# Kernel tuning notes

Hardware: AMD Instinct MI355X
Metric: run time of the kernel (lower is better)

## Reference

```python
import jax, jax.numpy as jnp
import numpy as np

UNITS = 1024
OUT_STEPS = 200
SEQ_LEN = 5
NUM_FEATURES = 1
BATCH = 4096


def _lstm_cell(x, h, c, kernel, recurrent_kernel, bias):
    # Keras LSTMCell: z = x@K + h@R + b, gates in order i, f, g(candidate), o
    z = x @ kernel + h @ recurrent_kernel + bias  # [B, 4U]
    i, f, g, o = jnp.split(z, 4, axis=-1)
    i = jax.nn.sigmoid(i)
    f = jax.nn.sigmoid(f)
    g = jnp.tanh(g)
    o = jax.nn.sigmoid(o)
    c_new = f * c + i * g
    h_new = o * jnp.tanh(c_new)
    return h_new, c_new


def setup_inputs() -> dict:
    key = jax.random.key(0)
    ks = jax.random.split(key, 8)
    s = 0.05  # modest init scale to keep gates unsaturated
    return {
        "inputs": jax.random.normal(ks[0], (BATCH, SEQ_LEN, NUM_FEATURES), jnp.float32),
        "kernel": jax.random.normal(ks[1], (NUM_FEATURES, 4 * UNITS), jnp.float32) * s,
        "recurrent_kernel": jax.random.normal(ks[2], (UNITS, 4 * UNITS), jnp.float32) * s,
        "bias": jax.random.normal(ks[3], (4 * UNITS,), jnp.float32) * s,
        "w1": jax.random.normal(ks[4], (UNITS, NUM_FEATURES), jnp.float32) * s,
        "b1": jax.random.normal(ks[5], (NUM_FEATURES,), jnp.float32) * s,
        "w2": jax.random.normal(ks[6], (NUM_FEATURES, NUM_FEATURES), jnp.float32) * s,
        "b2": jax.random.normal(ks[7], (NUM_FEATURES,), jnp.float32) * s,
    }


def reference(inputs, kernel, recurrent_kernel, bias, w1, b1, w2, b2):
    B = inputs.shape[0]
    h0 = jnp.zeros((B, UNITS), inputs.dtype)
    c0 = jnp.zeros((B, UNITS), inputs.dtype)

    # warmup: run LSTM over the input sequence (lax.scan over time)
    def warm_step(carry, x_t):
        h, c = carry
        h, c = _lstm_cell(x_t, h, c, kernel, recurrent_kernel, bias)
        return (h, c), None

    (h, c), _ = jax.lax.scan(warm_step, (h0, c0), jnp.swapaxes(inputs, 0, 1))
    pred0 = jax.nn.relu(h @ w1 + b1)  # first prediction: dense1 only (per warmup())

    def dec_step(carry, _):
        pred, h, c = carry
        h, c = _lstm_cell(pred, h, c, kernel, recurrent_kernel, bias)
        x = jax.nn.relu(h @ w1 + b1)
        pred = x @ w2 + b2
        return (pred, h, c), pred

    _, preds = jax.lax.scan(dec_step, (pred0, h, c), None, length=OUT_STEPS - 1)
    # preds: [T-1, B, F] -> stack with pred0 and transpose to [B, T, F]
    all_preds = jnp.concatenate([pred0[None], preds], axis=0)
    return jnp.transpose(all_preds, (1, 0, 2))
```

## Files before the change

kernel.cpp:

```cpp
#include <hip/hip_runtime.h>
#include <hip/hip_bf16.h>
#include <stdint.h>
#include <stddef.h>

#define B_SZ   4096
#define U_SZ   1024
#define SEQ    5
#define TSTEPS 200
#define STEPS  204

typedef __bf16 bf16_t;
typedef __bf16 bf16x8 __attribute__((ext_vector_type(8)));
typedef float  f32x4  __attribute__((ext_vector_type(4)));

#define AS1 __attribute__((address_space(1)))
#define AS3 __attribute__((address_space(3)))

#define LOAD_LDS16(gp, lp) \
    __builtin_amdgcn_global_load_lds((const AS1 unsigned int*)(gp), \
                                     (AS3 unsigned int*)(lp), 16, 0, 0)

__device__ __forceinline__ float fsig(float x) {
    return 1.0f / (1.0f + __expf(-x));
}
__device__ __forceinline__ float ftanh(float x) {
    x = fminf(fmaxf(x, -15.0f), 15.0f);
    float e = __expf(2.0f * x);
    return (e - 1.0f) / (e + 1.0f);
}

__global__ void pack_R(const float* __restrict__ R, bf16_t* __restrict__ Rp) {
    int idx = blockIdx.x * 256 + threadIdx.x;
    int e    = idx & 7;
    int slot = (idx >> 3) & 3;
    int c    = (idx >> 5) & 127;
    int kb   = (idx >> 12) & 31;
    int ub   = idx >> 17;
    int g  = (c >> 4) & 3;
    int wc = c >> 6;
    int cl = c & 15;
    int n  = g * 1024 + ub * 32 + wc * 16 + cl;
    int k  = kb * 32 + ((slot ^ ((c >> 1) & 3)) << 3) + e;
    Rp[idx] = (bf16_t)R[(size_t)k * 4096 + n];
}

__global__ __launch_bounds__(256, 2)
void lstm_step(const bf16_t* __restrict__ hin,
               bf16_t* __restrict__ hout,
               float* __restrict__ cst,
               const bf16_t* __restrict__ Rp,
               const float* __restrict__ Wx,
               const float* __restrict__ bias,
               const float* __restrict__ w1,
               const float* __restrict__ b1,
               const float* __restrict__ w2,
               const float* __restrict__ b2,
               const float* __restrict__ inputs,
               float* __restrict__ praw,
               float* __restrict__ out,
               int t)
{
    __shared__ __align__(16) bf16_t lsA[3][4096];
    __shared__ __align__(16) bf16_t lsB[3][2][4096];
    __shared__ float lsX[128];

    const int tid  = threadIdx.x;
    const int wave = tid >> 6;
    const int lane = tid & 63;
    const int p    = blockIdx.x;
    const int G    = blockIdx.y;
    const int l15  = lane & 15;
    const int quad = lane >> 4;
    const int rbase = (wave >> 1) * 64;
    const int wc    = wave & 1;
    const int a_kk32 = (((lane & 3) ^ ((lane >> 3) & 3)) << 3);
    const int sw32   = ((quad ^ ((l15 >> 1) & 3)) << 3);

    float*       pr_acc  = praw + (size_t)(t % 3) * B_SZ;
    const float* pr_read = praw + (size_t)((t + 2) % 3) * B_SZ;
    float*       pr_zero = praw + (size_t)((t + 1) % 3) * B_SZ;

    const bf16_t* Ap  = hin + (size_t)G * 128 * U_SZ;
    const bf16_t* Bp0 = Rp + (size_t)(2 * p) * 131072;
    const bf16_t* Bp1 = Bp0 + 131072;

    if (tid < 128) {
        int row = G * 128 + tid;
        float x;
        if (t < SEQ) {
            x = inputs[row * SEQ + t];
        } else {
            float x1 = fmaxf(pr_read[row] + b1[0], 0.f);
            x = (t == SEQ) ? x1 : x1 * w2[0] + b2[0];
            if (p == 0) out[(size_t)row * TSTEPS + (t - SEQ)] = x;
        }
        lsX[tid] = x;
        if (p == 0) pr_zero[row] = 0.f;
    }

    auto STAGE = [&](int ksrc, int buf) {
        #pragma unroll
        for (int i = 0; i < 2; ++i) {
            int brow = i * 64 + wave * 16;
            LOAD_LDS16(Ap + (size_t)(brow + (lane >> 2)) * U_SZ
                          + ksrc * 32 + a_kk32,
                       &lsA[buf][brow * 32]);
        }
        #pragma unroll
        for (int i = 0; i < 2; ++i) {
            int chunk = wave * 2 + i;
            LOAD_LDS16(Bp0 + (size_t)ksrc * 4096 + chunk * 512 + lane * 8,
                       &lsB[buf][0][chunk * 512]);
            LOAD_LDS16(Bp1 + (size_t)ksrc * 4096 + chunk * 512 + lane * 8,
                       &lsB[buf][1][chunk * 512]);
        }
    };

    STAGE(0, 0);
    STAGE(1, 1);

    f32x4 acc[2][4][4] = {};
    int bi = 0;

    for (int kb = 0; kb < 32; ++kb) {
        asm volatile("s_waitcnt vmcnt(6)" ::: "memory");
        __builtin_amdgcn_sched_barrier(0);
        __builtin_amdgcn_s_barrier();
        __builtin_amdgcn_sched_barrier(0);

        int bs = bi + 2; if (bs >= 3) bs -= 3;
        STAGE((kb + 2) & 31, bs);

        bf16x8 af[4], bfr[2][4];
        #pragma unroll
        for (int mi = 0; mi < 4; ++mi)
            af[mi] = *(const bf16x8*)
                &lsA[bi][(rbase + mi * 16 + l15) * 32 + sw32];
        #pragma unroll
        for (int T = 0; T < 2; ++T)
            #pragma unroll
            for (int ni = 0; ni < 4; ++ni)
                bfr[T][ni] = *(const bf16x8*)
                    &lsB[bi][T][(wc * 64 + ni * 16 + l15) * 32 + sw32];

        __builtin_amdgcn_s_setprio(1);
        #pragma unroll
        for (int T = 0; T < 2; ++T)
            #pragma unroll
            for (int mi = 0; mi < 4; ++mi)
                #pragma unroll
                for (int ni = 0; ni < 4; ++ni)
                    acc[T][mi][ni] = __builtin_amdgcn_mfma_f32_16x16x32_bf16(
                        af[mi], bfr[T][ni], acc[T][mi][ni], 0, 0, 0);
        __builtin_amdgcn_s_setprio(0);

        bi = bi + 1; if (bi >= 3) bi = 0;
    }

    int uu[2];
    uu[0] = (2 * p) * 32 + wc * 16 + l15;
    uu[1] = uu[0] + 32;
    float g_b[2][4], g_w[2][4], w1u[2];
    #pragma unroll
    for (int T = 0; T < 2; ++T) {
        #pragma unroll
        for (int g = 0; g < 4; ++g) {
            g_b[T][g] = bias[g * 1024 + uu[T]];
            g_w[T][g] = Wx[g * 1024 + uu[T]];
        }
        w1u[T] = w1[uu[T]];
    }
    const bool do_pred = (t >= SEQ - 1);

    #pragma unroll
    for (int mi = 0; mi < 4; ++mi) {
        #pragma unroll
        for (int r = 0; r < 4; ++r) {
            int rl   = rbase + mi * 16 + quad * 4 + r;
            int brow = G * 128 + rl;
            float xv = lsX[rl];
            float ps = 0.f;
            #pragma unroll
            for (int T = 0; T < 2; ++T) {
                float zi = acc[T][mi][0][r] + g_b[T][0] + xv * g_w[T][0];
                float zf = acc[T][mi][1][r] + g_b[T][1] + xv * g_w[T][1];
                float zg = acc[T][mi][2][r] + g_b[T][2] + xv * g_w[T][2];
                float zo = acc[T][mi][3][r] + g_b[T][3] + xv * g_w[T][3];
                float ig = fsig(zi), fg = fsig(zf);
                float gg = ftanh(zg), og = fsig(zo);
                size_t off = (size_t)brow * U_SZ + uu[T];
                float cn = fg * cst[off] + ig * gg;
                cst[off] = cn;
                float hv = og * ftanh(cn);
                hout[off] = (bf16_t)hv;
                ps += hv * w1u[T];
            }
            if (do_pred) {
                ps += __shfl_xor(ps, 1);
                ps += __shfl_xor(ps, 2);
                ps += __shfl_xor(ps, 4);
                ps += __shfl_xor(ps, 8);
                if (l15 == 0) atomicAdd(&pr_acc[brow], ps);
            }
        }
    }
}

__global__ void pred_final(const float* __restrict__ praw,
                           const float* __restrict__ b1,
                           const float* __restrict__ w2,
                           const float* __restrict__ b2,
                           float* __restrict__ out)
{
    int row = blockIdx.x * 256 + threadIdx.x;
    float x1 = fmaxf(praw[2 * B_SZ + row] + b1[0], 0.f);
    out[(size_t)row * TSTEPS + 199] = x1 * w2[0] + b2[0];
}

extern "C" void kernel_launch(void* const* d_in, const int* in_sizes, int n_in,
                              void* d_out, int out_size, void* d_ws, size_t ws_size,
                              hipStream_t stream) {
    const float* inputs = (const float*)d_in[0];
    const float* Wx     = (const float*)d_in[1];
    const float* R      = (const float*)d_in[2];
    const float* bias   = (const float*)d_in[3];
    const float* w1     = (const float*)d_in[4];
    const float* b1     = (const float*)d_in[5];
    const float* w2     = (const float*)d_in[6];
    const float* b2     = (const float*)d_in[7];
    float* out = (float*)d_out;

    char* ws = (char*)d_ws;
    const size_t RP_BYTES = (size_t)32 * 131072 * 2;
    const size_t H_BYTES  = (size_t)B_SZ * U_SZ * 2;
    const size_t C_BYTES  = (size_t)B_SZ * U_SZ * 4;
    bf16_t* Rp   = (bf16_t*)ws;                ws += RP_BYTES;
    bf16_t* h0   = (bf16_t*)ws;                ws += H_BYTES;
    bf16_t* h1   = (bf16_t*)ws;                ws += H_BYTES;
    float*  cbuf = (float*)ws;                 ws += C_BYTES;
    float*  praw = (float*)ws;                 ws += 3 * B_SZ * 4;
    bf16_t* hb[2] = {h0, h1};

    hipMemsetAsync(h0, 0, H_BYTES, stream);
    hipMemsetAsync(cbuf, 0, C_BYTES, stream);
    hipMemsetAsync(praw, 0, 3 * B_SZ * 4, stream);

    pack_R<<<16384, 256, 0, stream>>>(R, Rp);

    dim3 grid(16, 32);
    int cur = 0;
    for (int t = 0; t < STEPS; ++t) {
        lstm_step<<<grid, 256, 0, stream>>>(hb[cur], hb[1 - cur], cbuf, Rp,
                                            Wx, bias, w1, b1, w2, b2,
                                            inputs, praw, out, t);
        cur ^= 1;
    }
    pred_final<<<16, 256, 0, stream>>>(praw, b1, w2, b2, out);
}
```

Before: 9.719 ms.

## Register double-buffer LDS fragments and decouple A/B staging depths in GEMM loop

The K-loop now handles two k-blocks per iteration and keeps two register sets of A/B fragments. The next block's LDS reads are issued before the current block's MFMAs, so LDS latency overlaps matrix math. The B tiles drop from triple to double buffering in LDS, while A keeps three buffers and is prefetched one block further ahead. The vmcnt/lgkmcnt waits are reworked to match. This cuts LDS use and stalls between barrier and MFMA, at the cost of more vector registers and a more fragile wait-count schedule.

```diff
diff --git a/kernel.cpp b/kernel.cpp
--- a/kernel.cpp
+++ b/kernel.cpp
@@ -61,7 +61,7 @@
                int t)
 {
     __shared__ __align__(16) bf16_t lsA[3][4096];
-    __shared__ __align__(16) bf16_t lsB[3][2][4096];
+    __shared__ __align__(16) bf16_t lsB[2][2][4096];
     __shared__ float lsX[128];
 
     const int tid  = threadIdx.x;
@@ -98,63 +98,91 @@
         if (p == 0) pr_zero[row] = 0.f;
     }
 
-    auto STAGE = [&](int ksrc, int buf) {
+    auto STAGE_A = [&](int ksrc, int abuf) {
         #pragma unroll
         for (int i = 0; i < 2; ++i) {
             int brow = i * 64 + wave * 16;
             LOAD_LDS16(Ap + (size_t)(brow + (lane >> 2)) * U_SZ
                           + ksrc * 32 + a_kk32,
-                       &lsA[buf][brow * 32]);
-        }
+                       &lsA[abuf][brow * 32]);
+        }
+    };
+    auto STAGE_B = [&](int ksrc, int bbuf) {
         #pragma unroll
         for (int i = 0; i < 2; ++i) {
             int chunk = wave * 2 + i;
             LOAD_LDS16(Bp0 + (size_t)ksrc * 4096 + chunk * 512 + lane * 8,
-                       &lsB[buf][0][chunk * 512]);
+                       &lsB[bbuf][0][chunk * 512]);
             LOAD_LDS16(Bp1 + (size_t)ksrc * 4096 + chunk * 512 + lane * 8,
-                       &lsB[buf][1][chunk * 512]);
+                       &lsB[bbuf][1][chunk * 512]);
         }
     };
 
-    STAGE(0, 0);
-    STAGE(1, 1);
+#define DSREAD(abuf, bbuf, af, b0, b1)                                        \
+    {   _Pragma("unroll")                                                     \
+        for (int mi = 0; mi < 4; ++mi)                                        \
+            af[mi] = *(const bf16x8*)                                         \
+                &lsA[abuf][(rbase + mi * 16 + l15) * 32 + sw32];              \
+        _Pragma("unroll")                                                     \
+        for (int ni = 0; ni < 4; ++ni) {                                      \
+            b0[ni] = *(const bf16x8*)                                         \
+                &lsB[bbuf][0][(wc * 64 + ni * 16 + l15) * 32 + sw32];         \
+            b1[ni] = *(const bf16x8*)                                         \
+                &lsB[bbuf][1][(wc * 64 + ni * 16 + l15) * 32 + sw32];         \
+        } }
+
+#define MFMA32(af, b0, b1)                                                    \
+    {   __builtin_amdgcn_s_setprio(1);                                        \
+        _Pragma("unroll")                                                     \
+        for (int mi = 0; mi < 4; ++mi)                                        \
+            _Pragma("unroll")                                                 \
+            for (int ni = 0; ni < 4; ++ni)                                    \
+                acc[0][mi][ni] = __builtin_amdgcn_mfma_f32_16x16x32_bf16(     \
+                    af[mi], b0[ni], acc[0][mi][ni], 0, 0, 0);                 \
+        _Pragma("unroll")                                                     \
+        for (int mi = 0; mi < 4; ++mi)                                        \
+            _Pragma("unroll")                                                 \
+            for (int ni = 0; ni < 4; ++ni)                                    \
+                acc[1][mi][ni] = __builtin_amdgcn_mfma_f32_16x16x32_bf16(     \
+                    af[mi], b1[ni], acc[1][mi][ni], 0, 0, 0);                 \
+        __builtin_amdgcn_s_setprio(0); }
+
+#define SYNC_HALF                                                             \
+    asm volatile("s_waitcnt vmcnt(2) lgkmcnt(0)" ::: "memory");               \
+    __builtin_amdgcn_sched_barrier(0);                                        \
+    __builtin_amdgcn_s_barrier();                                             \
+    __builtin_amdgcn_sched_barrier(0);
+
+    STAGE_B(0, 0); STAGE_B(1, 1);
+    STAGE_A(0, 0); STAGE_A(1, 1); STAGE_A(2, 2);
 
     f32x4 acc[2][4][4] = {};
-    int bi = 0;
-
-    for (int kb = 0; kb < 32; ++kb) {
-        asm volatile("s_waitcnt vmcnt(6)" ::: "memory");
-        __builtin_amdgcn_sched_barrier(0);
-        __builtin_amdgcn_s_barrier();
-        __builtin_amdgcn_sched_barrier(0);
-
-        int bs = bi + 2; if (bs >= 3) bs -= 3;
-        STAGE((kb + 2) & 31, bs);
-
-        bf16x8 af[4], bfr[2][4];
-        #pragma unroll
-        for (int mi = 0; mi < 4; ++mi)
-            af[mi] = *(const bf16x8*)
-                &lsA[bi][(rbase + mi * 16 + l15) * 32 + sw32];
-        #pragma unroll
-        for (int T = 0; T < 2; ++T)
-            #pragma unroll
-            for (int ni = 0; ni < 4; ++ni)
-                bfr[T][ni] = *(const bf16x8*)
-                    &lsB[bi][T][(wc * 64 + ni * 16 + l15) * 32 + sw32];
-
-        __builtin_amdgcn_s_setprio(1);
-        #pragma unroll
-        for (int T = 0; T < 2; ++T)
-            #pragma unroll
-            for (int mi = 0; mi < 4; ++mi)
-                #pragma unroll
-                for (int ni = 0; ni < 4; ++ni)
-                    acc[T][mi][ni] = __builtin_amdgcn_mfma_f32_16x16x32_bf16(
-                        af[mi], bfr[T][ni], acc[T][mi][ni], 0, 0, 0);
-        __builtin_amdgcn_s_setprio(0);
-
-        bi = bi + 1; if (bi >= 3) bi = 0;
+    bf16x8 afE[4], bE0[4], bE1[4];
+    bf16x8 afO[4], bO0[4], bO1[4];
+
+    asm volatile("s_waitcnt vmcnt(2)" ::: "memory");
+    __builtin_amdgcn_s_barrier();
+    DSREAD(0, 0, afE, bE0, bE1);
+
+    int a = 0;
+    #pragma clang loop unroll(disable)
+    for (int kb = 0; kb < 32; kb += 2) {
+        const int a1 = (a + 1 == 3) ? 0 : a + 1;
+        const int a2 = (a1 + 1 == 3) ? 0 : a1 + 1;
+
+        SYNC_HALF;
+        STAGE_B((kb + 2) & 31, 0);
+        STAGE_A((kb + 3) & 31, a);
+        DSREAD(a1, 1, afO, bO0, bO1);
+        MFMA32(afE, bE0, bE1);
+
+        SYNC_HALF;
+        STAGE_B((kb + 3) & 31, 1);
+        STAGE_A((kb + 4) & 31, a1);
+        if (kb < 30) DSREAD(a2, 0, afE, bE0, bE1);
+        MFMA32(afO, bO0, bO1);
+
+        a = a2;
     }
 
     int uu[2];
```

Result: no change. 9.904 ms (+1.9%).

## Halve per-block N tile, double grid, and remap blocks for XCD-local L2 reuse

Applied to the files above, without the earlier changes.

Each block now computes one 32-unit slice of R instead of two, so the grid doubles to 1024 blocks and launch bounds rise to 4 blocks per CU. The B buffer drops to double buffering with staggered A/B staging, and lsX is replaced by a per-wave register read through shuffles. Block IDs are swizzled so that blocks on the same XCD share h rows and R columns, which should improve L2 hit rates. Smaller tiles lower arithmetic intensity per A load and add extra A traffic in exchange for more occupancy and parallelism.

```diff
diff --git a/kernel.cpp b/kernel.cpp
--- a/kernel.cpp
+++ b/kernel.cpp
@@ -44,7 +44,7 @@
     Rp[idx] = (bf16_t)R[(size_t)k * 4096 + n];
 }
 
-__global__ __launch_bounds__(256, 2)
+__global__ __launch_bounds__(256, 4)
 void lstm_step(const bf16_t* __restrict__ hin,
                bf16_t* __restrict__ hout,
                float* __restrict__ cst,
@@ -61,14 +61,16 @@
                int t)
 {
     __shared__ __align__(16) bf16_t lsA[3][4096];
-    __shared__ __align__(16) bf16_t lsB[3][2][4096];
-    __shared__ float lsX[128];
+    __shared__ __align__(16) bf16_t lsB[2][4096];
 
     const int tid  = threadIdx.x;
     const int wave = tid >> 6;
     const int lane = tid & 63;
-    const int p    = blockIdx.x;
-    const int G    = blockIdx.y;
+    const int bid  = blockIdx.x + 32 * blockIdx.y;
+    const int xcd  = bid & 7;
+    const int j    = bid >> 3;
+    const int p    = (xcd & 3) * 8 + (j & 7);
+    const int G    = (xcd >> 2) * 16 + (j >> 3);
     const int l15  = lane & 15;
     const int quad = lane >> 4;
     const int rbase = (wave >> 1) * 64;
@@ -80,96 +82,89 @@
     const float* pr_read = praw + (size_t)((t + 2) % 3) * B_SZ;
     float*       pr_zero = praw + (size_t)((t + 1) % 3) * B_SZ;
 
-    const bf16_t* Ap  = hin + (size_t)G * 128 * U_SZ;
-    const bf16_t* Bp0 = Rp + (size_t)(2 * p) * 131072;
-    const bf16_t* Bp1 = Bp0 + 131072;
-
-    if (tid < 128) {
-        int row = G * 128 + tid;
+    const bf16_t* Ap = hin + (size_t)G * 128 * U_SZ;
+    const bf16_t* Bp = Rp + (size_t)p * 131072;
+
+    auto STAGE_A = [&](int ksrc, int abuf) {
+        #pragma unroll
+        for (int i = 0; i < 2; ++i) {
+            int brow = i * 64 + wave * 16;
+            LOAD_LDS16(Ap + (size_t)(brow + (lane >> 2)) * U_SZ
+                          + ksrc * 32 + a_kk32,
+                       &lsA[abuf][brow * 32]);
+        }
+    };
+    auto STAGE_B = [&](int ksrc, int bbuf) {
+        #pragma unroll
+        for (int i = 0; i < 2; ++i) {
+            int chunk = wave * 2 + i;
+            LOAD_LDS16(Bp + (size_t)ksrc * 4096 + chunk * 512 + lane * 8,
+                       &lsB[bbuf][chunk * 512]);
+        }
+    };
+
+    STAGE_A(0, 0); STAGE_B(0, 0); STAGE_A(1, 1);
+
+    float xw;
+    {
+        int row = G * 128 + rbase + lane;
         float x;
         if (t < SEQ) {
             x = inputs[row * SEQ + t];
         } else {
             float x1 = fmaxf(pr_read[row] + b1[0], 0.f);
             x = (t == SEQ) ? x1 : x1 * w2[0] + b2[0];
-            if (p == 0) out[(size_t)row * TSTEPS + (t - SEQ)] = x;
-        }
-        lsX[tid] = x;
-        if (p == 0) pr_zero[row] = 0.f;
-    }
-
-    auto STAGE = [&](int ksrc, int buf) {
-        #pragma unroll
-        for (int i = 0; i < 2; ++i) {
-            int brow = i * 64 + wave * 16;
-            LOAD_LDS16(Ap + (size_t)(brow + (lane >> 2)) * U_SZ
-                          + ksrc * 32 + a_kk32,
-                       &lsA[buf][brow * 32]);
-        }
-        #pragma unroll
-        for (int i = 0; i < 2; ++i) {
-            int chunk = wave * 2 + i;
-            LOAD_LDS16(Bp0 + (size_t)ksrc * 4096 + chunk * 512 + lane * 8,
-                       &lsB[buf][0][chunk * 512]);
-            LOAD_LDS16(Bp1 + (size_t)ksrc * 4096 + chunk * 512 + lane * 8,
-                       &lsB[buf][1][chunk * 512]);
-        }
-    };
-
-    STAGE(0, 0);
-    STAGE(1, 1);
-
-    f32x4 acc[2][4][4] = {};
-    int bi = 0;
-
+            if (p == 0 && (wave & 1) == 0)
+                out[(size_t)row * TSTEPS + (t - SEQ)] = x;
+        }
+        xw = x;
+        if (p == 0 && (wave & 1) == 0) pr_zero[row] = 0.f;
+    }
+
+    f32x4 acc[4][4] = {};
+    int ap = 0;
+
+    #pragma clang loop unroll(disable)
     for (int kb = 0; kb < 32; ++kb) {
-        asm volatile("s_waitcnt vmcnt(6)" ::: "memory");
+        asm volatile("s_waitcnt vmcnt(2)" ::: "memory");
         __builtin_amdgcn_sched_barrier(0);
         __builtin_amdgcn_s_barrier();
         __builtin_amdgcn_sched_barrier(0);
 
-        int bs = bi + 2; if (bs >= 3) bs -= 3;
-        STAGE((kb + 2) & 31, bs);
-
-        bf16x8 af[4], bfr[2][4];
+        if (kb < 31) STAGE_B(kb + 1, (kb + 1) & 1);
+        int ap2 = ap + 2; if (ap2 >= 3) ap2 -= 3;
+        if (kb < 30) STAGE_A(kb + 2, ap2);
+
+        bf16x8 af[4], bfr[4];
         #pragma unroll
         for (int mi = 0; mi < 4; ++mi)
             af[mi] = *(const bf16x8*)
-                &lsA[bi][(rbase + mi * 16 + l15) * 32 + sw32];
-        #pragma unroll
-        for (int T = 0; T < 2; ++T)
+                &lsA[ap][(rbase + mi * 16 + l15) * 32 + sw32];
+        #pragma unroll
+        for (int ni = 0; ni < 4; ++ni)
+            bfr[ni] = *(const bf16x8*)
+                &lsB[kb & 1][(wc * 64 + ni * 16 + l15) * 32 + sw32];
+
+        __builtin_amdgcn_s_setprio(1);
+        #pragma unroll
+        for (int mi = 0; mi < 4; ++mi)
             #pragma unroll
             for (int ni = 0; ni < 4; ++ni)
-                bfr[T][ni] = *(const bf16x8*)
-                    &lsB[bi][T][(wc * 64 + ni * 16 + l15) * 32 + sw32];
-
-        __builtin_amdgcn_s_setprio(1);
-        #pragma unroll
-        for (int T = 0; T < 2; ++T)
-            #pragma unroll
-            for (int mi = 0; mi < 4; ++mi)
-                #pragma unroll
-                for (int ni = 0; ni < 4; ++ni)
-                    acc[T][mi][ni] = __builtin_amdgcn_mfma_f32_16x16x32_bf16(
-                        af[mi], bfr[T][ni], acc[T][mi][ni], 0, 0, 0);
+                acc[mi][ni] = __builtin_amdgcn_mfma_f32_16x16x32_bf16(
+                    af[mi], bfr[ni], acc[mi][ni], 0, 0, 0);
         __builtin_amdgcn_s_setprio(0);
 
-        bi = bi + 1; if (bi >= 3) bi = 0;
-    }
-
-    int uu[2];
-    uu[0] = (2 * p) * 32 + wc * 16 + l15;
-    uu[1] = uu[0] + 32;
-    float g_b[2][4], g_w[2][4], w1u[2];
+        ap = ap + 1; if (ap >= 3) ap = 0;
+    }
+
+    const int uu = p * 32 + wc * 16 + l15;
+    float g_b[4], g_w[4];
     #pragma unroll
-    for (int T = 0; T < 2; ++T) {
-        #pragma unroll
-        for (int g = 0; g < 4; ++g) {
-            g_b[T][g] = bias[g * 1024 + uu[T]];
-            g_w[T][g] = Wx[g * 1024 + uu[T]];
-        }
-        w1u[T] = w1[uu[T]];
-    }
+    for (int g = 0; g < 4; ++g) {
+        g_b[g] = bias[g * 1024 + uu];
+        g_w[g] = Wx[g * 1024 + uu];
+    }
+    const float w1u = w1[uu];
     const bool do_pred = (t >= SEQ - 1);
 
     #pragma unroll
@@ -178,23 +173,19 @@
         for (int r = 0; r < 4; ++r) {
             int rl   = rbase + mi * 16 + quad * 4 + r;
             int brow = G * 128 + rl;
-            float xv = lsX[rl];
-            float ps = 0.f;
-            #pragma unroll
-            for (int T = 0; T < 2; ++T) {
-                float zi = acc[T][mi][0][r] + g_b[T][0] + xv * g_w[T][0];
-                float zf = acc[T][mi][1][r] + g_b[T][1] + xv * g_w[T][1];
-                float zg = acc[T][mi][2][r] + g_b[T][2] + xv * g_w[T][2];
-                float zo = acc[T][mi][3][r] + g_b[T][3] + xv * g_w[T][3];
-                float ig = fsig(zi), fg = fsig(zf);
-                float gg = ftanh(zg), og = fsig(zo);
-                size_t off = (size_t)brow * U_SZ + uu[T];
-                float cn = fg * cst[off] + ig * gg;
-                cst[off] = cn;
-                float hv = og * ftanh(cn);
-                hout[off] = (bf16_t)hv;
-                ps += hv * w1u[T];
-            }
+            float xv = __shfl(xw, mi * 16 + quad * 4 + r);
+            float zi = acc[mi][0][r] + g_b[0] + xv * g_w[0];
+            float zf = acc[mi][1][r] + g_b[1] + xv * g_w[1];
+            float zg = acc[mi][2][r] + g_b[2] + xv * g_w[2];
+            float zo = acc[mi][3][r] + g_b[3] + xv * g_w[3];
+            float ig = fsig(zi), fg = fsig(zf);
+            float gg = ftanh(zg), og = fsig(zo);
+            size_t off = (size_t)brow * U_SZ + uu;
+            float cn = fg * cst[off] + ig * gg;
+            cst[off] = cn;
+            float hv = og * ftanh(cn);
+            hout[off] = (bf16_t)hv;
+            float ps = hv * w1u;
             if (do_pred) {
                 ps += __shfl_xor(ps, 1);
                 ps += __shfl_xor(ps, 2);
@@ -247,7 +238,7 @@
 
     pack_R<<<16384, 256, 0, stream>>>(R, Rp);
 
-    dim3 grid(16, 32);
+    dim3 grid(32, 32);
     int cur = 0;
     for (int t = 0; t < STEPS; ++t) {
         lstm_step<<<grid, 256, 0, stream>>>(hb[cur], hb[1 - cur], cbuf, Rp,
```

New measurement: 9.173 ms. 5.6% less time.
